# Performance work log

Measured on AMD Instinct MI355X. Metric: run time of the kernel, lower is better.

The kernel has to match this reference:

```python
import jax, jax.numpy as jnp
import numpy as np

B, MSG, H, D, N = 64, 64, 512, 512, 2048


def setup_inputs() -> dict:
    key = jax.random.key(0)
    ks = jax.random.split(key, 20)
    s = 0.02
    return {
        "message": jax.random.normal(ks[0], (B, MSG), jnp.float32),
        "state": jax.random.normal(ks[1], (B, H), jnp.float32),
        "image": jax.random.normal(ks[2], (B, H), jnp.float32),
        "class_descriptors": jax.random.normal(ks[3], (N, D), jnp.float32),
        # GRUCell params (torch layout: gates ordered r, z, n)
        "w_ih": jax.random.normal(ks[4], (3 * H, MSG), jnp.float32) * s,
        "w_hh": jax.random.normal(ks[5], (3 * H, H), jnp.float32) * s,
        "b_ih": jax.random.normal(ks[6], (3 * H,), jnp.float32) * s,
        "b_hh": jax.random.normal(ks[7], (3 * H,), jnp.float32) * s,
        "w_stop": jax.random.normal(ks[8], (1, H), jnp.float32) * s,
        "b_stop": jax.random.normal(ks[9], (1,), jnp.float32) * s,
        "w_y1": jax.random.normal(ks[10], (H, H + D), jnp.float32) * s,
        "b_y1": jax.random.normal(ks[11], (H,), jnp.float32) * s,
        "w_y2": jax.random.normal(ks[12], (1, H), jnp.float32) * s,
        "b_y2": jax.random.normal(ks[13], (1,), jnp.float32) * s,
        "w_state": jax.random.normal(ks[14], (H, H), jnp.float32) * s,
        "b_state": jax.random.normal(ks[15], (H,), jnp.float32) * s,
        "w_desc": jax.random.normal(ks[16], (H, D), jnp.float32) * s,  # no bias
        "w_msg": jax.random.normal(ks[17], (MSG, H), jnp.float32) * s,
        "b_msg": jax.random.normal(ks[18], (MSG,), jnp.float32) * s,
    }


def _gru_cell(x, h, w_ih, w_hh, b_ih, b_hh):
    gi = x @ w_ih.T + b_ih  # [B, 3H]
    gh = h @ w_hh.T + b_hh
    i_r, i_z, i_n = jnp.split(gi, 3, axis=1)
    h_r, h_z, h_n = jnp.split(gh, 3, axis=1)
    r = jax.nn.sigmoid(i_r + h_r)
    z = jax.nn.sigmoid(i_z + h_z)
    n = jnp.tanh(i_n + r * h_n)
    return (1.0 - z) * n + z * h


def reference(message, state, image, class_descriptors,
              w_ih, w_hh, b_ih, b_hh, w_stop, b_stop,
              w_y1, b_y1, w_y2, b_y2, w_state, b_state,
              w_desc, w_msg, b_msg):
    b, h = state.shape
    n, d = class_descriptors.shape

    new_state = _gru_cell(message, state, w_ih, w_hh, b_ih, b_hh)  # [B, H]
    stop_dist = jax.nn.sigmoid(new_state @ w_stop.T + b_stop)  # [B, 1]
    stop_bit = jax.lax.stop_gradient(jnp.round(stop_dist))  # eval-mode path

    # build_state_descriptor_pairs (faithful to torch view semantics,
    # including the (B, H, N) -> (B*N, H) interleaved reshape of pair_left)
    pair_left = jnp.broadcast_to(new_state[:, :, None], (b, h, n)).reshape(b * n, h)
    pair_right = jnp.broadcast_to(class_descriptors[None], (b, n, d)).reshape(b * n, d)
    pairs = jnp.concatenate([pair_left, pair_right], axis=1)  # [B*N, H+D]

    y = jnp.clip(pairs @ w_y1.T + b_y1, 0.0, None)  # relu, [B*N, H]
    y = (y @ w_y2.T + b_y2).reshape(b, -1)  # [B, N]
    y_scores = jax.lax.stop_gradient(jax.nn.softmax(y, axis=1))

    # reweight_descriptors: softmax-weighted sum over descriptors
    descriptor_influence = jnp.einsum('bn,nd->bd', y_scores, class_descriptors)

    message_state = jnp.tanh(new_state @ w_state.T + b_state
                             + descriptor_influence @ w_desc.T)
    message_dist = jax.nn.sigmoid(message_state @ w_msg.T + b_msg)  # [B, MSG]
    outp_msg = jax.lax.stop_gradient(jnp.round(message_dist))

    return stop_bit, stop_dist, outp_msg, message_dist, y
```

## Files before the change

kernel.cpp:

```cpp
#include <hip/hip_runtime.h>
#include <hip/hip_bf16.h>


__device__ __forceinline__ float sigm(float x) { return 1.0f / (1.0f + expf(-x)); }

__device__ __forceinline__ void stage_pad68(float* dst, const float* src, int c) {
  *(float4*)&dst[(c >> 4) * 68 + (c & 15) * 4] = *(const float4*)&src[c * 4];
}

__global__ __launch_bounds__(512) void gru_kernel(
    const float* __restrict__ msg, const float* __restrict__ st,
    const float* __restrict__ w_ih, const float* __restrict__ w_hh,
    const float* __restrict__ b_ih, const float* __restrict__ b_hh,
    float* __restrict__ ns, float* __restrict__ nsT) {
  const int h = blockIdx.x;
  const int t = threadIdx.x;
  __shared__ __align__(16) float sHr[544], sHz[544], sHn[544];
  __shared__ __align__(16) float sIr[64], sIz[64], sIn[64];
  if (t < 128)      stage_pad68(sHr, w_hh + h * 512, t);
  else if (t < 256) stage_pad68(sHz, w_hh + (h + 512) * 512, t - 128);
  else if (t < 384) stage_pad68(sHn, w_hh + (h + 1024) * 512, t - 256);
  else if (t < 400) ((float4*)sIr)[t - 384] = ((const float4*)(w_ih + h * 64))[t - 384];
  else if (t < 416) ((float4*)sIz)[t - 400] = ((const float4*)(w_ih + (h + 512) * 64))[t - 400];
  else if (t < 432) ((float4*)sIn)[t - 416] = ((const float4*)(w_ih + (h + 1024) * 64))[t - 416];
  __syncthreads();
  const int bi = t >> 3, kg = t & 7;
  float pr = 0.f, pz = 0.f, pin = 0.f, phn = 0.f;
  {
    const float* mrow = msg + bi * 64 + kg * 8;
    const float* ir = &sIr[kg * 8];
    const float* iz = &sIz[kg * 8];
    const float* in_ = &sIn[kg * 8];
    #pragma unroll
    for (int i = 0; i < 2; ++i) {
      float4 x = *(const float4*)&mrow[i * 4];
      float4 wr = *(const float4*)&ir[i * 4];
      float4 wz = *(const float4*)&iz[i * 4];
      float4 wn = *(const float4*)&in_[i * 4];
      pr = fmaf(x.x, wr.x, pr); pr = fmaf(x.y, wr.y, pr); pr = fmaf(x.z, wr.z, pr); pr = fmaf(x.w, wr.w, pr);
      pz = fmaf(x.x, wz.x, pz); pz = fmaf(x.y, wz.y, pz); pz = fmaf(x.z, wz.z, pz); pz = fmaf(x.w, wz.w, pz);
      pin = fmaf(x.x, wn.x, pin); pin = fmaf(x.y, wn.y, pin); pin = fmaf(x.z, wn.z, pin); pin = fmaf(x.w, wn.w, pin);
    }
  }
  {
    const float* srow = st + bi * 512 + kg * 64;
    const float* hr = &sHr[kg * 68];
    const float* hz = &sHz[kg * 68];
    const float* hn = &sHn[kg * 68];
    #pragma unroll
    for (int i = 0; i < 16; ++i) {
      float4 x = *(const float4*)&srow[i * 4];
      float4 wr = *(const float4*)&hr[i * 4];
      float4 wz = *(const float4*)&hz[i * 4];
      float4 wn = *(const float4*)&hn[i * 4];
      pr = fmaf(x.x, wr.x, pr); pr = fmaf(x.y, wr.y, pr); pr = fmaf(x.z, wr.z, pr); pr = fmaf(x.w, wr.w, pr);
      pz = fmaf(x.x, wz.x, pz); pz = fmaf(x.y, wz.y, pz); pz = fmaf(x.z, wz.z, pz); pz = fmaf(x.w, wz.w, pz);
      phn = fmaf(x.x, wn.x, phn); phn = fmaf(x.y, wn.y, phn); phn = fmaf(x.z, wn.z, phn); phn = fmaf(x.w, wn.w, phn);
    }
  }
  pr += __shfl_xor(pr, 1, 8); pr += __shfl_xor(pr, 2, 8); pr += __shfl_xor(pr, 4, 8);
  pz += __shfl_xor(pz, 1, 8); pz += __shfl_xor(pz, 2, 8); pz += __shfl_xor(pz, 4, 8);
  pin += __shfl_xor(pin, 1, 8); pin += __shfl_xor(pin, 2, 8); pin += __shfl_xor(pin, 4, 8);
  phn += __shfl_xor(phn, 1, 8); phn += __shfl_xor(phn, 2, 8); phn += __shfl_xor(phn, 4, 8);
  if ((t & 7) == 0) {
    float r = sigm(pr + b_ih[h] + b_hh[h]);
    float z = sigm(pz + b_ih[h + 512] + b_hh[h + 512]);
    float n = tanhf(pin + b_ih[h + 1024] + r * (phn + b_hh[h + 1024]));
    float hp = st[bi * 512 + h];
    float v = (1.0f - z) * n + z * hp;
    ns[bi * 512 + h] = v;
    nsT[h * 64 + bi] = v;
  }
}

__global__ __launch_bounds__(512) void stopws1_kernel(
    const float* __restrict__ w_y1, float* __restrict__ ws1,
    const float* __restrict__ ns, const float* __restrict__ w_stop,
    const float* __restrict__ b_stop, float* __restrict__ out_bit,
    float* __restrict__ out_dist) {
  const int t = threadIdx.x;
  if (blockIdx.x < 64) {
    const int j = blockIdx.x * 8 + (t >> 6);
    const int lane = t & 63;
    const float* row = w_y1 + j * 1024 + lane * 8;
    float4 a = *(const float4*)&row[0];
    float4 b = *(const float4*)&row[4];
    float acc = a.x + a.y + a.z + a.w + b.x + b.y + b.z + b.w;
    #pragma unroll
    for (int m = 1; m < 64; m <<= 1) acc += __shfl_xor(acc, m, 64);
    if (lane == 0) ws1[j] = acc;
  } else {
    const int bi = t >> 3, kg = t & 7;
    const float* row = ns + bi * 512 + kg * 64;
    const float* wrow = w_stop + kg * 64;
    float acc = 0.f;
    #pragma unroll
    for (int i = 0; i < 16; ++i) {
      float4 r = *(const float4*)&row[i * 4];
      float4 w = *(const float4*)&wrow[i * 4];
      acc = fmaf(r.x, w.x, acc); acc = fmaf(r.y, w.y, acc);
      acc = fmaf(r.z, w.z, acc); acc = fmaf(r.w, w.w, acc);
    }
    acc += __shfl_xor(acc, 1, 8); acc += __shfl_xor(acc, 2, 8); acc += __shfl_xor(acc, 4, 8);
    if ((t & 7) == 0) {
      float sd = sigm(acc + b_stop[0]);
      out_dist[bi] = sd;
      out_bit[bi] = rintf(sd);
    }
  }
}

#define GBK 16
__global__ __launch_bounds__(256) void g_kernel(
    const float* __restrict__ desc, const float* __restrict__ w_y1,
    const float* __restrict__ b_y1, const float* __restrict__ nsT,
    const float* __restrict__ ws1, const float* __restrict__ w_y2,
    float* __restrict__ yp) {
  __shared__ __align__(16) float As[GBK][64];
  __shared__ __align__(16) float Bs[GBK][64];
  __shared__ __align__(16) float sV[16][66];
  __shared__ __align__(16) float sW1[64], sW2[64];
  const int rr0 = blockIdx.x * 64;
  const int j0 = blockIdx.y * 64;
  const int tid = threadIdx.x;
  const int tm = (tid >> 4) * 4;
  const int tn = (tid & 15) * 4;
  const int lm = tid >> 2;
  const int lkq = (tid & 3) * 4;
  {
    const int q = tid >> 4, pos = (tid & 15) * 4;
    *(float4*)&sV[q][pos] = *(const float4*)&nsT[((rr0 >> 2) + q) * 64 + pos];
  }
  if (tid < 64) { sW1[tid] = ws1[j0 + tid]; sW2[tid] = w_y2[j0 + tid]; }
  float acc[4][4] = {};
  const float* aptr = desc + (rr0 + lm) * 512 + lkq;
  const float* bptr = w_y1 + (j0 + lm) * 1024 + 512 + lkq;
  float4 av = *(const float4*)aptr;
  float4 bv = *(const float4*)bptr;
  for (int k0 = 0; k0 < 512; k0 += GBK) {
    __syncthreads();
    As[lkq + 0][lm] = av.x; As[lkq + 1][lm] = av.y;
    As[lkq + 2][lm] = av.z; As[lkq + 3][lm] = av.w;
    Bs[lkq + 0][lm] = bv.x; Bs[lkq + 1][lm] = bv.y;
    Bs[lkq + 2][lm] = bv.z; Bs[lkq + 3][lm] = bv.w;
    __syncthreads();
    if (k0 + GBK < 512) {
      av = *(const float4*)(aptr + k0 + GBK);
      bv = *(const float4*)(bptr + k0 + GBK);
    }
    #pragma unroll
    for (int k = 0; k < GBK; ++k) {
      float4 a = *(const float4*)&As[k][tm];
      float4 b = *(const float4*)&Bs[k][tn];
      acc[0][0] = fmaf(a.x, b.x, acc[0][0]); acc[0][1] = fmaf(a.x, b.y, acc[0][1]);
      acc[0][2] = fmaf(a.x, b.z, acc[0][2]); acc[0][3] = fmaf(a.x, b.w, acc[0][3]);
      acc[1][0] = fmaf(a.y, b.x, acc[1][0]); acc[1][1] = fmaf(a.y, b.y, acc[1][1]);
      acc[1][2] = fmaf(a.y, b.z, acc[1][2]); acc[1][3] = fmaf(a.y, b.w, acc[1][3]);
      acc[2][0] = fmaf(a.z, b.x, acc[2][0]); acc[2][1] = fmaf(a.z, b.y, acc[2][1]);
      acc[2][2] = fmaf(a.z, b.z, acc[2][2]); acc[2][3] = fmaf(a.z, b.w, acc[2][3]);
      acc[3][0] = fmaf(a.w, b.x, acc[3][0]); acc[3][1] = fmaf(a.w, b.y, acc[3][1]);
      acc[3][2] = fmaf(a.w, b.z, acc[3][2]); acc[3][3] = fmaf(a.w, b.w, acc[3][3]);
    }
  }
  {
    float4 by = *(const float4*)&b_y1[j0 + tn];
    #pragma unroll
    for (int i = 0; i < 4; ++i) {
      acc[i][0] += by.x; acc[i][1] += by.y; acc[i][2] += by.z; acc[i][3] += by.w;
    }
  }
  const float4 w1 = *(const float4*)&sW1[tn];
  const float4 w2 = *(const float4*)&sW2[tn];
  const int vrow = tid >> 4;
  float* ypb = yp + blockIdx.y * 131072 + rr0 + tm;
  for (int bi = 0; bi < 64; ++bi) {
    const float v = sV[vrow][bi];
    float p0 = fmaf(w2.x, fmaxf(fmaf(v, w1.x, acc[0][0]), 0.f),
               fmaf(w2.y, fmaxf(fmaf(v, w1.y, acc[0][1]), 0.f),
               fmaf(w2.z, fmaxf(fmaf(v, w1.z, acc[0][2]), 0.f),
                    w2.w * fmaxf(fmaf(v, w1.w, acc[0][3]), 0.f))));
    float p1 = fmaf(w2.x, fmaxf(fmaf(v, w1.x, acc[1][0]), 0.f),
               fmaf(w2.y, fmaxf(fmaf(v, w1.y, acc[1][1]), 0.f),
               fmaf(w2.z, fmaxf(fmaf(v, w1.z, acc[1][2]), 0.f),
                    w2.w * fmaxf(fmaf(v, w1.w, acc[1][3]), 0.f))));
    float p2 = fmaf(w2.x, fmaxf(fmaf(v, w1.x, acc[2][0]), 0.f),
               fmaf(w2.y, fmaxf(fmaf(v, w1.y, acc[2][1]), 0.f),
               fmaf(w2.z, fmaxf(fmaf(v, w1.z, acc[2][2]), 0.f),
                    w2.w * fmaxf(fmaf(v, w1.w, acc[2][3]), 0.f))));
    float p3 = fmaf(w2.x, fmaxf(fmaf(v, w1.x, acc[3][0]), 0.f),
               fmaf(w2.y, fmaxf(fmaf(v, w1.y, acc[3][1]), 0.f),
               fmaf(w2.z, fmaxf(fmaf(v, w1.z, acc[3][2]), 0.f),
                    w2.w * fmaxf(fmaf(v, w1.w, acc[3][3]), 0.f))));
    p0 += __shfl_xor(p0, 1, 16); p0 += __shfl_xor(p0, 2, 16); p0 += __shfl_xor(p0, 4, 16); p0 += __shfl_xor(p0, 8, 16);
    p1 += __shfl_xor(p1, 1, 16); p1 += __shfl_xor(p1, 2, 16); p1 += __shfl_xor(p1, 4, 16); p1 += __shfl_xor(p1, 8, 16);
    p2 += __shfl_xor(p2, 1, 16); p2 += __shfl_xor(p2, 2, 16); p2 += __shfl_xor(p2, 4, 16); p2 += __shfl_xor(p2, 8, 16);
    p3 += __shfl_xor(p3, 1, 16); p3 += __shfl_xor(p3, 2, 16); p3 += __shfl_xor(p3, 4, 16); p3 += __shfl_xor(p3, 8, 16);
    if ((tid & 15) == 0) *(float4*)&ypb[bi * 2048] = make_float4(p0, p1, p2, p3);
  }
}

__global__ __launch_bounds__(256) void softmax_kernel(
    const float* __restrict__ yp, const float* __restrict__ b_y2,
    float* __restrict__ scores, float* __restrict__ out_y) {
  const int bi = blockIdx.x;
  const int t = threadIdx.x;
  __shared__ float sy[2048];
  __shared__ float red[256];
  const float b = b_y2[0];
  float lmax = -3.0e38f;
  for (int i = t; i < 2048; i += 256) {
    const float* p = yp + bi * 2048 + i;
    float v = b + p[0] + p[131072] + p[262144] + p[393216]
                + p[524288] + p[655360] + p[786432] + p[917504];
    sy[i] = v;
    out_y[bi * 2048 + i] = v;
    lmax = fmaxf(lmax, v);
  }
  red[t] = lmax;
  __syncthreads();
  for (int s = 128; s > 0; s >>= 1) {
    if (t < s) red[t] = fmaxf(red[t], red[t + s]);
    __syncthreads();
  }
  const float mx = red[0];
  __syncthreads();
  float lsum = 0.0f;
  for (int i = t; i < 2048; i += 256) {
    float e = expf(sy[i] - mx);
    sy[i] = e;
    lsum += e;
  }
  red[t] = lsum;
  __syncthreads();
  for (int s = 128; s > 0; s >>= 1) {
    if (t < s) red[t] += red[t + s];
    __syncthreads();
  }
  const float inv = 1.0f / red[0];
  for (int i = t; i < 2048; i += 256) scores[bi * 2048 + i] = sy[i] * inv;
}

__global__ __launch_bounds__(256) void di_part_kernel(
    const float* __restrict__ scores, const float* __restrict__ desc,
    float* __restrict__ dp) {
  __shared__ __align__(16) float sS[64][64];
  __shared__ __align__(16) float sD[64][64];
  const int d0 = blockIdx.x * 64;
  const int n0 = blockIdx.y * 64;
  const int tid = threadIdx.x;
  {
    const int bi = tid >> 2;
    #pragma unroll
    for (int i = 0; i < 4; ++i) {
      const int kq = (tid & 3) * 4 + i * 16;
      float4 av = *(const float4*)&scores[bi * 2048 + n0 + kq];
      sS[kq + 0][bi] = av.x; sS[kq + 1][bi] = av.y;
      sS[kq + 2][bi] = av.z; sS[kq + 3][bi] = av.w;
    }
  }
  {
    #pragma unroll
    for (int i = 0; i < 4; ++i) {
      const int nn = (tid >> 4) + i * 16;
      const int dq = (tid & 15) * 4;
      *(float4*)&sD[nn][dq] = *(const float4*)&desc[(n0 + nn) * 512 + d0 + dq];
    }
  }
  __syncthreads();
  const int bi0 = (tid >> 4) * 4;
  const int dd0 = (tid & 15) * 4;
  float acc[4][4] = {};
  #pragma unroll 8
  for (int nn = 0; nn < 64; ++nn) {
    float4 a = *(const float4*)&sS[nn][bi0];
    float4 b = *(const float4*)&sD[nn][dd0];
    acc[0][0] = fmaf(a.x, b.x, acc[0][0]); acc[0][1] = fmaf(a.x, b.y, acc[0][1]);
    acc[0][2] = fmaf(a.x, b.z, acc[0][2]); acc[0][3] = fmaf(a.x, b.w, acc[0][3]);
    acc[1][0] = fmaf(a.y, b.x, acc[1][0]); acc[1][1] = fmaf(a.y, b.y, acc[1][1]);
    acc[1][2] = fmaf(a.y, b.z, acc[1][2]); acc[1][3] = fmaf(a.y, b.w, acc[1][3]);
    acc[2][0] = fmaf(a.z, b.x, acc[2][0]); acc[2][1] = fmaf(a.z, b.y, acc[2][1]);
    acc[2][2] = fmaf(a.z, b.z, acc[2][2]); acc[2][3] = fmaf(a.z, b.w, acc[2][3]);
    acc[3][0] = fmaf(a.w, b.x, acc[3][0]); acc[3][1] = fmaf(a.w, b.y, acc[3][1]);
    acc[3][2] = fmaf(a.w, b.z, acc[3][2]); acc[3][3] = fmaf(a.w, b.w, acc[3][3]);
  }
  float* base = dp + blockIdx.y * 32768;
  #pragma unroll
  for (int i = 0; i < 4; ++i)
    #pragma unroll
    for (int j = 0; j < 4; ++j)
      base[(bi0 + i) * 512 + d0 + dd0 + j] = acc[i][j];
}

__global__ __launch_bounds__(512) void di_reduce_kernel(
    const float* __restrict__ dp, float* __restrict__ di) {
  const int idx = blockIdx.x * 512 + threadIdx.x;
  float acc = 0.0f;
  #pragma unroll 8
  for (int c = 0; c < 32; ++c) acc += dp[c * 32768 + idx];
  di[idx] = acc;
}

__global__ __launch_bounds__(512) void ms_kernel(
    const float* __restrict__ ns, const float* __restrict__ di,
    const float* __restrict__ w_state, const float* __restrict__ b_state,
    const float* __restrict__ w_desc, float* __restrict__ ms) {
  const int hj = blockIdx.x;
  const int t = threadIdx.x;
  __shared__ __align__(16) float sWs[544], sWd[544];
  if (t < 128)      stage_pad68(sWs, w_state + hj * 512, t);
  else if (t < 256) stage_pad68(sWd, w_desc + hj * 512, t - 128);
  __syncthreads();
  const int bi = t >> 3, kg = t & 7;
  const float* nr = ns + bi * 512 + kg * 64;
  const float* dr = di + bi * 512 + kg * 64;
  const float* wsp = &sWs[kg * 68];
  const float* wdp = &sWd[kg * 68];
  float acc = 0.f;
  #pragma unroll
  for (int i = 0; i < 16; ++i) {
    float4 a = *(const float4*)&nr[i * 4];
    float4 w = *(const float4*)&wsp[i * 4];
    float4 b = *(const float4*)&dr[i * 4];
    float4 u = *(const float4*)&wdp[i * 4];
    acc = fmaf(a.x, w.x, acc); acc = fmaf(a.y, w.y, acc);
    acc = fmaf(a.z, w.z, acc); acc = fmaf(a.w, w.w, acc);
    acc = fmaf(b.x, u.x, acc); acc = fmaf(b.y, u.y, acc);
    acc = fmaf(b.z, u.z, acc); acc = fmaf(b.w, u.w, acc);
  }
  acc += __shfl_xor(acc, 1, 8); acc += __shfl_xor(acc, 2, 8); acc += __shfl_xor(acc, 4, 8);
  if ((t & 7) == 0) ms[bi * 512 + hj] = tanhf(acc + b_state[hj]);
}

__global__ __launch_bounds__(512) void msg_kernel(
    const float* __restrict__ ms, const float* __restrict__ w_msg,
    const float* __restrict__ b_msg, float* __restrict__ out_msg,
    float* __restrict__ out_msgdist) {
  const int m = blockIdx.x;
  const int t = threadIdx.x;
  __shared__ __align__(16) float sW[544];
  if (t < 128) stage_pad68(sW, w_msg + m * 512, t);
  __syncthreads();
  const int bi = t >> 3, kg = t & 7;
  const float* row = ms + bi * 512 + kg * 64;
  const float* wp = &sW[kg * 68];
  float acc = 0.f;
  #pragma unroll
  for (int i = 0; i < 16; ++i) {
    float4 a = *(const float4*)&row[i * 4];
    float4 w = *(const float4*)&wp[i * 4];
    acc = fmaf(a.x, w.x, acc); acc = fmaf(a.y, w.y, acc);
    acc = fmaf(a.z, w.z, acc); acc = fmaf(a.w, w.w, acc);
  }
  acc += __shfl_xor(acc, 1, 8); acc += __shfl_xor(acc, 2, 8); acc += __shfl_xor(acc, 4, 8);
  if ((t & 7) == 0) {
    float md = sigm(acc + b_msg[m]);
    out_msgdist[bi * 64 + m] = md;
    out_msg[bi * 64 + m] = rintf(md);
  }
}

extern "C" void kernel_launch(void* const* d_in, const int* in_sizes, int n_in,
                              void* d_out, int out_size, void* d_ws, size_t ws_size,
                              hipStream_t stream) {
  (void)in_sizes; (void)n_in; (void)out_size; (void)ws_size;
  const float* message = (const float*)d_in[0];
  const float* state   = (const float*)d_in[1];
  const float* desc    = (const float*)d_in[3];
  const float* w_ih    = (const float*)d_in[4];
  const float* w_hh    = (const float*)d_in[5];
  const float* b_ih    = (const float*)d_in[6];
  const float* b_hh    = (const float*)d_in[7];
  const float* w_stop  = (const float*)d_in[8];
  const float* b_stop  = (const float*)d_in[9];
  const float* w_y1    = (const float*)d_in[10];
  const float* b_y1    = (const float*)d_in[11];
  const float* w_y2    = (const float*)d_in[12];
  const float* b_y2    = (const float*)d_in[13];
  const float* w_state = (const float*)d_in[14];
  const float* b_state = (const float*)d_in[15];
  const float* w_desc  = (const float*)d_in[16];
  const float* w_msg   = (const float*)d_in[17];
  const float* b_msg   = (const float*)d_in[18];

  float* out = (float*)d_out;
  float* out_stopbit  = out;
  float* out_stopdist = out + 64;
  float* out_msg      = out + 128;
  float* out_msgdist  = out + 4224;
  float* out_y        = out + 8320;

  char* ws = (char*)d_ws;
  float* ns     = (float*)(ws);
  float* nsT    = (float*)(ws + 131072);
  float* ws1    = (float*)(ws + 262144);
  float* yp     = (float*)(ws + 270336);
  float* scores = (float*)(ws + 4988928);
  float* di     = (float*)(ws + 5513216);
  float* ms     = (float*)(ws + 5644288);

  gru_kernel<<<512, 512, 0, stream>>>(message, state, w_ih, w_hh, b_ih, b_hh, ns, nsT);
  stopws1_kernel<<<65, 512, 0, stream>>>(w_y1, ws1, ns, w_stop, b_stop, out_stopbit, out_stopdist);
  g_kernel<<<dim3(32, 8), 256, 0, stream>>>(desc, w_y1, b_y1, nsT, ws1, w_y2, yp);
  softmax_kernel<<<64, 256, 0, stream>>>(yp, b_y2, scores, out_y);
  di_part_kernel<<<dim3(8, 32), 256, 0, stream>>>(scores, desc, yp);
  di_reduce_kernel<<<64, 512, 0, stream>>>(yp, di);
  ms_kernel<<<512, 512, 0, stream>>>(ns, di, w_state, b_state, w_desc, ms);
  msg_kernel<<<64, 512, 0, stream>>>(ms, w_msg, b_msg, out_msg, out_msgdist);
}
```

Baseline: 213.8 us.

## Split G GEMM from y epilogue, fold ws1 into GRU kernel, full-row y kernel

Merges the w_y1 row-sum (ws1) blocks into the GRU launch, which removes one kernel. The GEMM now writes the full G matrix [2048x512] with smaller 32x64 tiles and two blocks per CU. A new ystop kernel computes each y column over all 512 hidden units per descriptor row, so the partial yp buffers and the 8-way partial reduction in softmax are no longer needed. In exchange, G (4 MB) makes an extra round trip through global memory, and the y epilogue now needs 2048 blocks.

```diff
diff --git a/kernel.cpp b/kernel.cpp
--- a/kernel.cpp
+++ b/kernel.cpp
@@ -1,5 +1,4 @@
 #include <hip/hip_runtime.h>
-#include <hip/hip_bf16.h>
 
 
 __device__ __forceinline__ float sigm(float x) { return 1.0f / (1.0f + expf(-x)); }
@@ -8,13 +7,26 @@
   *(float4*)&dst[(c >> 4) * 68 + (c & 15) * 4] = *(const float4*)&src[c * 4];
 }
 
-__global__ __launch_bounds__(512) void gru_kernel(
+__global__ __launch_bounds__(512) void gruws1_kernel(
     const float* __restrict__ msg, const float* __restrict__ st,
     const float* __restrict__ w_ih, const float* __restrict__ w_hh,
     const float* __restrict__ b_ih, const float* __restrict__ b_hh,
-    float* __restrict__ ns, float* __restrict__ nsT) {
+    const float* __restrict__ w_y1,
+    float* __restrict__ ns, float* __restrict__ nsT, float* __restrict__ ws1) {
+  const int t = threadIdx.x;
+  if (blockIdx.x >= 512) {
+    const int j = (blockIdx.x - 512) * 8 + (t >> 6);
+    const int lane = t & 63;
+    const float* row = w_y1 + j * 1024 + lane * 8;
+    float4 a = *(const float4*)&row[0];
+    float4 b = *(const float4*)&row[4];
+    float acc = a.x + a.y + a.z + a.w + b.x + b.y + b.z + b.w;
+    #pragma unroll
+    for (int m = 1; m < 64; m <<= 1) acc += __shfl_xor(acc, m, 64);
+    if (lane == 0) ws1[j] = acc;
+    return;
+  }
   const int h = blockIdx.x;
-  const int t = threadIdx.x;
   __shared__ __align__(16) float sHr[544], sHz[544], sHn[544];
   __shared__ __align__(16) float sIr[64], sIz[64], sIn[64];
   if (t < 128)      stage_pad68(sHr, w_hh + h * 512, t);
@@ -73,145 +85,129 @@
   }
 }
 
-__global__ __launch_bounds__(512) void stopws1_kernel(
-    const float* __restrict__ w_y1, float* __restrict__ ws1,
+__global__ __launch_bounds__(256, 2) void g_kernel(
+    const float* __restrict__ desc, const float* __restrict__ w_y1,
+    const float* __restrict__ b_y1, float* __restrict__ G) {
+  __shared__ __align__(16) float As[32 * 33];
+  __shared__ __align__(16) float Bs[32 * 68];
+  const int rr0 = blockIdx.x * 32;
+  const int j0 = blockIdx.y * 64;
+  const int t = threadIdx.x;
+  const int lrow = t >> 3;
+  const int lk4 = (t & 7) * 4;
+  const int tm2 = (t >> 4) * 2;
+  const int tn4 = (t & 15) * 4;
+  const float* aptr = desc + (rr0 + lrow) * 512 + lk4;
+  const float* bptr0 = w_y1 + (j0 + lrow) * 1024 + 512 + lk4;
+  const float* bptr1 = bptr0 + 32 * 1024;
+  float4 av = *(const float4*)aptr;
+  float4 bv0 = *(const float4*)bptr0;
+  float4 bv1 = *(const float4*)bptr1;
+  float acc[2][4] = {};
+  for (int k0 = 0; k0 < 512; k0 += 32) {
+    __syncthreads();
+    As[(lk4 + 0) * 33 + lrow] = av.x; As[(lk4 + 1) * 33 + lrow] = av.y;
+    As[(lk4 + 2) * 33 + lrow] = av.z; As[(lk4 + 3) * 33 + lrow] = av.w;
+    Bs[(lk4 + 0) * 68 + lrow] = bv0.x; Bs[(lk4 + 1) * 68 + lrow] = bv0.y;
+    Bs[(lk4 + 2) * 68 + lrow] = bv0.z; Bs[(lk4 + 3) * 68 + lrow] = bv0.w;
+    Bs[(lk4 + 0) * 68 + lrow + 32] = bv1.x; Bs[(lk4 + 1) * 68 + lrow + 32] = bv1.y;
+    Bs[(lk4 + 2) * 68 + lrow + 32] = bv1.z; Bs[(lk4 + 3) * 68 + lrow + 32] = bv1.w;
+    __syncthreads();
+    if (k0 + 32 < 512) {
+      av = *(const float4*)(aptr + k0 + 32);
+      bv0 = *(const float4*)(bptr0 + k0 + 32);
+      bv1 = *(const float4*)(bptr1 + k0 + 32);
+    }
+    #pragma unroll
+    for (int k = 0; k < 32; ++k) {
+      float a0 = As[k * 33 + tm2];
+      float a1 = As[k * 33 + tm2 + 1];
+      float4 b = *(const float4*)&Bs[k * 68 + tn4];
+      acc[0][0] = fmaf(a0, b.x, acc[0][0]); acc[0][1] = fmaf(a0, b.y, acc[0][1]);
+      acc[0][2] = fmaf(a0, b.z, acc[0][2]); acc[0][3] = fmaf(a0, b.w, acc[0][3]);
+      acc[1][0] = fmaf(a1, b.x, acc[1][0]); acc[1][1] = fmaf(a1, b.y, acc[1][1]);
+      acc[1][2] = fmaf(a1, b.z, acc[1][2]); acc[1][3] = fmaf(a1, b.w, acc[1][3]);
+    }
+  }
+  float4 by = *(const float4*)&b_y1[j0 + tn4];
+  float4 r0 = make_float4(acc[0][0] + by.x, acc[0][1] + by.y, acc[0][2] + by.z, acc[0][3] + by.w);
+  float4 r1 = make_float4(acc[1][0] + by.x, acc[1][1] + by.y, acc[1][2] + by.z, acc[1][3] + by.w);
+  *(float4*)&G[(rr0 + tm2) * 512 + j0 + tn4] = r0;
+  *(float4*)&G[(rr0 + tm2 + 1) * 512 + j0 + tn4] = r1;
+}
+
+__global__ __launch_bounds__(256) void ystop_kernel(
+    const float* __restrict__ nsT, const float* __restrict__ ws1,
+    const float* __restrict__ G, const float* __restrict__ w_y2,
+    const float* __restrict__ b_y2, float* __restrict__ yf,
     const float* __restrict__ ns, const float* __restrict__ w_stop,
     const float* __restrict__ b_stop, float* __restrict__ out_bit,
     float* __restrict__ out_dist) {
   const int t = threadIdx.x;
-  if (blockIdx.x < 64) {
-    const int j = blockIdx.x * 8 + (t >> 6);
-    const int lane = t & 63;
-    const float* row = w_y1 + j * 1024 + lane * 8;
-    float4 a = *(const float4*)&row[0];
-    float4 b = *(const float4*)&row[4];
-    float acc = a.x + a.y + a.z + a.w + b.x + b.y + b.z + b.w;
-    #pragma unroll
-    for (int m = 1; m < 64; m <<= 1) acc += __shfl_xor(acc, m, 64);
-    if (lane == 0) ws1[j] = acc;
-  } else {
-    const int bi = t >> 3, kg = t & 7;
-    const float* row = ns + bi * 512 + kg * 64;
-    const float* wrow = w_stop + kg * 64;
+  if (blockIdx.x == 2048) {
+    const int bi = t >> 2, kg = t & 3;
+    const float* row = ns + bi * 512 + kg * 128;
+    const float* wrow = w_stop + kg * 128;
     float acc = 0.f;
     #pragma unroll
-    for (int i = 0; i < 16; ++i) {
+    for (int i = 0; i < 32; ++i) {
       float4 r = *(const float4*)&row[i * 4];
       float4 w = *(const float4*)&wrow[i * 4];
       acc = fmaf(r.x, w.x, acc); acc = fmaf(r.y, w.y, acc);
       acc = fmaf(r.z, w.z, acc); acc = fmaf(r.w, w.w, acc);
     }
-    acc += __shfl_xor(acc, 1, 8); acc += __shfl_xor(acc, 2, 8); acc += __shfl_xor(acc, 4, 8);
-    if ((t & 7) == 0) {
+    acc += __shfl_xor(acc, 1, 4); acc += __shfl_xor(acc, 2, 4);
+    if (kg == 0) {
       float sd = sigm(acc + b_stop[0]);
       out_dist[bi] = sd;
       out_bit[bi] = rintf(sd);
     }
-  }
-}
-
-#define GBK 16
-__global__ __launch_bounds__(256) void g_kernel(
-    const float* __restrict__ desc, const float* __restrict__ w_y1,
-    const float* __restrict__ b_y1, const float* __restrict__ nsT,
-    const float* __restrict__ ws1, const float* __restrict__ w_y2,
-    float* __restrict__ yp) {
-  __shared__ __align__(16) float As[GBK][64];
-  __shared__ __align__(16) float Bs[GBK][64];
-  __shared__ __align__(16) float sV[16][66];
-  __shared__ __align__(16) float sW1[64], sW2[64];
-  const int rr0 = blockIdx.x * 64;
-  const int j0 = blockIdx.y * 64;
-  const int tid = threadIdx.x;
-  const int tm = (tid >> 4) * 4;
-  const int tn = (tid & 15) * 4;
-  const int lm = tid >> 2;
-  const int lkq = (tid & 3) * 4;
-  {
-    const int q = tid >> 4, pos = (tid & 15) * 4;
-    *(float4*)&sV[q][pos] = *(const float4*)&nsT[((rr0 >> 2) + q) * 64 + pos];
-  }
-  if (tid < 64) { sW1[tid] = ws1[j0 + tid]; sW2[tid] = w_y2[j0 + tid]; }
-  float acc[4][4] = {};
-  const float* aptr = desc + (rr0 + lm) * 512 + lkq;
-  const float* bptr = w_y1 + (j0 + lm) * 1024 + 512 + lkq;
-  float4 av = *(const float4*)aptr;
-  float4 bv = *(const float4*)bptr;
-  for (int k0 = 0; k0 < 512; k0 += GBK) {
-    __syncthreads();
-    As[lkq + 0][lm] = av.x; As[lkq + 1][lm] = av.y;
-    As[lkq + 2][lm] = av.z; As[lkq + 3][lm] = av.w;
-    Bs[lkq + 0][lm] = bv.x; Bs[lkq + 1][lm] = bv.y;
-    Bs[lkq + 2][lm] = bv.z; Bs[lkq + 3][lm] = bv.w;
-    __syncthreads();
-    if (k0 + GBK < 512) {
-      av = *(const float4*)(aptr + k0 + GBK);
-      bv = *(const float4*)(bptr + k0 + GBK);
-    }
-    #pragma unroll
-    for (int k = 0; k < GBK; ++k) {
-      float4 a = *(const float4*)&As[k][tm];
-      float4 b = *(const float4*)&Bs[k][tn];
-      acc[0][0] = fmaf(a.x, b.x, acc[0][0]); acc[0][1] = fmaf(a.x, b.y, acc[0][1]);
-      acc[0][2] = fmaf(a.x, b.z, acc[0][2]); acc[0][3] = fmaf(a.x, b.w, acc[0][3]);
-      acc[1][0] = fmaf(a.y, b.x, acc[1][0]); acc[1][1] = fmaf(a.y, b.y, acc[1][1]);
-      acc[1][2] = fmaf(a.y, b.z, acc[1][2]); acc[1][3] = fmaf(a.y, b.w, acc[1][3]);
-      acc[2][0] = fmaf(a.z, b.x, acc[2][0]); acc[2][1] = fmaf(a.z, b.y, acc[2][1]);
-      acc[2][2] = fmaf(a.z, b.z, acc[2][2]); acc[2][3] = fmaf(a.z, b.w, acc[2][3]);
-      acc[3][0] = fmaf(a.w, b.x, acc[3][0]); acc[3][1] = fmaf(a.w, b.y, acc[3][1]);
-      acc[3][2] = fmaf(a.w, b.z, acc[3][2]); acc[3][3] = fmaf(a.w, b.w, acc[3][3]);
-    }
-  }
-  {
-    float4 by = *(const float4*)&b_y1[j0 + tn];
-    #pragma unroll
-    for (int i = 0; i < 4; ++i) {
-      acc[i][0] += by.x; acc[i][1] += by.y; acc[i][2] += by.z; acc[i][3] += by.w;
-    }
-  }
-  const float4 w1 = *(const float4*)&sW1[tn];
-  const float4 w2 = *(const float4*)&sW2[tn];
-  const int vrow = tid >> 4;
-  float* ypb = yp + blockIdx.y * 131072 + rr0 + tm;
-  for (int bi = 0; bi < 64; ++bi) {
-    const float v = sV[vrow][bi];
-    float p0 = fmaf(w2.x, fmaxf(fmaf(v, w1.x, acc[0][0]), 0.f),
-               fmaf(w2.y, fmaxf(fmaf(v, w1.y, acc[0][1]), 0.f),
-               fmaf(w2.z, fmaxf(fmaf(v, w1.z, acc[0][2]), 0.f),
-                    w2.w * fmaxf(fmaf(v, w1.w, acc[0][3]), 0.f))));
-    float p1 = fmaf(w2.x, fmaxf(fmaf(v, w1.x, acc[1][0]), 0.f),
-               fmaf(w2.y, fmaxf(fmaf(v, w1.y, acc[1][1]), 0.f),
-               fmaf(w2.z, fmaxf(fmaf(v, w1.z, acc[1][2]), 0.f),
-                    w2.w * fmaxf(fmaf(v, w1.w, acc[1][3]), 0.f))));
-    float p2 = fmaf(w2.x, fmaxf(fmaf(v, w1.x, acc[2][0]), 0.f),
-               fmaf(w2.y, fmaxf(fmaf(v, w1.y, acc[2][1]), 0.f),
-               fmaf(w2.z, fmaxf(fmaf(v, w1.z, acc[2][2]), 0.f),
-                    w2.w * fmaxf(fmaf(v, w1.w, acc[2][3]), 0.f))));
-    float p3 = fmaf(w2.x, fmaxf(fmaf(v, w1.x, acc[3][0]), 0.f),
-               fmaf(w2.y, fmaxf(fmaf(v, w1.y, acc[3][1]), 0.f),
-               fmaf(w2.z, fmaxf(fmaf(v, w1.z, acc[3][2]), 0.f),
-                    w2.w * fmaxf(fmaf(v, w1.w, acc[3][3]), 0.f))));
-    p0 += __shfl_xor(p0, 1, 16); p0 += __shfl_xor(p0, 2, 16); p0 += __shfl_xor(p0, 4, 16); p0 += __shfl_xor(p0, 8, 16);
-    p1 += __shfl_xor(p1, 1, 16); p1 += __shfl_xor(p1, 2, 16); p1 += __shfl_xor(p1, 4, 16); p1 += __shfl_xor(p1, 8, 16);
-    p2 += __shfl_xor(p2, 1, 16); p2 += __shfl_xor(p2, 2, 16); p2 += __shfl_xor(p2, 4, 16); p2 += __shfl_xor(p2, 8, 16);
-    p3 += __shfl_xor(p3, 1, 16); p3 += __shfl_xor(p3, 2, 16); p3 += __shfl_xor(p3, 4, 16); p3 += __shfl_xor(p3, 8, 16);
-    if ((tid & 15) == 0) *(float4*)&ypb[bi * 2048] = make_float4(p0, p1, p2, p3);
+    return;
+  }
+  const int rr = blockIdx.x;
+  __shared__ __align__(16) float sG[512], sW1[512], sW2[512];
+  __shared__ float sp[4 * 72];
+  if (t < 128) {
+    ((float4*)sG)[t] = ((const float4*)(G + rr * 512))[t];
+    ((float4*)sW2)[t] = ((const float4*)w_y2)[t];
+  } else {
+    ((float4*)sW1)[t - 128] = ((const float4*)ws1)[t - 128];
+  }
+  __syncthreads();
+  const int bi = t & 63, jq = t >> 6;
+  const float v = nsT[(rr >> 2) * 64 + bi];
+  float acc = 0.0f;
+  const float* g = sG + jq * 128;
+  const float* w1 = sW1 + jq * 128;
+  const float* w2 = sW2 + jq * 128;
+  #pragma unroll 4
+  for (int j = 0; j < 128; j += 4) {
+    float4 gv = *(const float4*)&g[j];
+    float4 a1 = *(const float4*)&w1[j];
+    float4 a2 = *(const float4*)&w2[j];
+    acc = fmaf(a2.x, fmaxf(fmaf(v, a1.x, gv.x), 0.0f), acc);
+    acc = fmaf(a2.y, fmaxf(fmaf(v, a1.y, gv.y), 0.0f), acc);
+    acc = fmaf(a2.z, fmaxf(fmaf(v, a1.z, gv.z), 0.0f), acc);
+    acc = fmaf(a2.w, fmaxf(fmaf(v, a1.w, gv.w), 0.0f), acc);
+  }
+  sp[jq * 72 + bi] = acc;
+  __syncthreads();
+  if (t < 64) {
+    float y = sp[t] + sp[72 + t] + sp[144 + t] + sp[216 + t] + b_y2[0];
+    yf[t * 2048 + rr] = y;
   }
 }
 
 __global__ __launch_bounds__(256) void softmax_kernel(
-    const float* __restrict__ yp, const float* __restrict__ b_y2,
-    float* __restrict__ scores, float* __restrict__ out_y) {
+    const float* __restrict__ yf, float* __restrict__ scores,
+    float* __restrict__ out_y) {
   const int bi = blockIdx.x;
   const int t = threadIdx.x;
   __shared__ float sy[2048];
   __shared__ float red[256];
-  const float b = b_y2[0];
   float lmax = -3.0e38f;
   for (int i = t; i < 2048; i += 256) {
-    const float* p = yp + bi * 2048 + i;
-    float v = b + p[0] + p[131072] + p[262144] + p[393216]
-                + p[524288] + p[655360] + p[786432] + p[917504];
+    float v = yf[bi * 2048 + i];
     sy[i] = v;
     out_y[bi * 2048 + i] = v;
     lmax = fmaxf(lmax, v);
@@ -393,17 +389,20 @@
   float* ns     = (float*)(ws);
   float* nsT    = (float*)(ws + 131072);
   float* ws1    = (float*)(ws + 262144);
-  float* yp     = (float*)(ws + 270336);
-  float* scores = (float*)(ws + 4988928);
-  float* di     = (float*)(ws + 5513216);
-  float* ms     = (float*)(ws + 5644288);
-
-  gru_kernel<<<512, 512, 0, stream>>>(message, state, w_ih, w_hh, b_ih, b_hh, ns, nsT);
-  stopws1_kernel<<<65, 512, 0, stream>>>(w_y1, ws1, ns, w_stop, b_stop, out_stopbit, out_stopdist);
-  g_kernel<<<dim3(32, 8), 256, 0, stream>>>(desc, w_y1, b_y1, nsT, ws1, w_y2, yp);
-  softmax_kernel<<<64, 256, 0, stream>>>(yp, b_y2, scores, out_y);
-  di_part_kernel<<<dim3(8, 32), 256, 0, stream>>>(scores, desc, yp);
-  di_reduce_kernel<<<64, 512, 0, stream>>>(yp, di);
+  float* G      = (float*)(ws + 264192);
+  float* yf     = (float*)(ws + 4458496);
+  float* scores = (float*)(ws + 4982784);
+  float* di     = (float*)(ws + 5507072);
+  float* ms     = (float*)(ws + 5638144);
+
+  gruws1_kernel<<<576, 512, 0, stream>>>(message, state, w_ih, w_hh, b_ih, b_hh,
+                                         w_y1, ns, nsT, ws1);
+  g_kernel<<<dim3(64, 8), 256, 0, stream>>>(desc, w_y1, b_y1, G);
+  ystop_kernel<<<2049, 256, 0, stream>>>(nsT, ws1, G, w_y2, b_y2, yf,
+                                         ns, w_stop, b_stop, out_stopbit, out_stopdist);
+  softmax_kernel<<<64, 256, 0, stream>>>(yf, scores, out_y);
+  di_part_kernel<<<dim3(8, 32), 256, 0, stream>>>(scores, desc, G);
+  di_reduce_kernel<<<64, 512, 0, stream>>>(G, di);
   ms_kernel<<<512, 512, 0, stream>>>(ns, di, w_state, b_state, w_desc, ms);
   msg_kernel<<<64, 512, 0, stream>>>(ms, w_msg, b_msg, out_msg, out_msgdist);
 }
```

Result: faster. 194.6 us (-9.0%).
